# Kernel tuning notes

Hardware: AMD Instinct MI355X
Metric: run time of the kernel (lower is better)

Reference implementation:

```python
import jax, jax.numpy as jnp
import numpy as np

DECAY = 0.99
EPS = 1e-06


def setup_inputs() -> dict:
    key = jax.random.key(0)
    k1, k2, k3 = jax.random.split(key, 3)
    B, S, D, K = 8, 8192, 256, 2048
    x = jax.random.normal(k1, (B, S, D), dtype=jnp.float32)
    embed = jax.random.normal(k2, (K, D), dtype=jnp.float32)
    cluster_size = jnp.ones((K,), dtype=jnp.float32)
    embed_avg = jax.random.normal(k3, (K, D), dtype=jnp.float32)
    return {"x": x, "embed": embed, "cluster_size": cluster_size, "embed_avg": embed_avg}


def reference(x, embed, cluster_size, embed_avg):
    # x: [B, S, D]; embed/embed_avg: [K, D]; cluster_size: [K]
    B, S, D = x.shape
    K = embed.shape[0]
    xf = x.reshape(-1, D)  # [N, D]
    dist = (
        jnp.sum(xf * xf, axis=1, keepdims=True)
        - 2.0 * (xf @ embed.T)
        + jnp.sum(embed * embed, axis=1)
    )
    embed_ind_flat = jnp.argmin(dist, axis=-1)  # [N]
    quantize = embed[embed_ind_flat].reshape(B, S, D)
    embed_ind = embed_ind_flat.reshape(B, S)

    # EMA updates (training branch). one_hot.sum(0) == per-code counts,
    # one_hot.T @ x == per-code feature sums; use segment_sum (no NxK one-hot).
    counts = jax.ops.segment_sum(
        jnp.ones((B * S,), dtype=jnp.float32), embed_ind_flat, num_segments=K
    )
    embed_sum = jax.ops.segment_sum(xf, embed_ind_flat, num_segments=K)  # [K, D]
    new_cluster_size = cluster_size * DECAY + (1.0 - DECAY) * counts
    new_embed_avg = embed_avg * DECAY + (1.0 - DECAY) * embed_sum
    total = new_cluster_size.sum()
    smoothed = (new_cluster_size + EPS) / (total + EPS * K) * total  # laplace smoothing
    new_embed = new_embed_avg / smoothed[:, None]
    return quantize, embed_ind, new_cluster_size, new_embed_avg, new_embed
```

## Files before the change

kernel.cpp:

```cpp
#include <hip/hip_runtime.h>
#include <hip/hip_bf16.h>
#include <float.h>

#define DECAY 0.99f
#define OMD   0.01f
#define EPSF  1e-6f

constexpr int Bb = 8, Ss = 8192, Dd = 256, Kk = 2048;
constexpr int Nn = Bb * Ss;

constexpr long OUT_QUANT = 0;
constexpr long OUT_IND   = (long)Nn * Dd;
constexpr long OUT_NCS   = OUT_IND + Nn;
constexpr long OUT_NEA   = OUT_NCS + Kk;
constexpr long OUT_NE    = OUT_NEA + (long)Kk * Dd;

constexpr long WS_COUNTS = 0;
constexpr long WS_TOTAL  = 2048;
constexpr long WS_EE     = 2112;
constexpr long WS_BIG    = 4160;
constexpr int  PARTS     = 8;

typedef __attribute__((ext_vector_type(8))) short short8;
typedef __attribute__((ext_vector_type(4))) float floatx4;

#define WINDOW 0.0625f

__device__ __forceinline__ void gl_lds(const ushort* g, ushort* l)
{
    __builtin_amdgcn_global_load_lds(
        (const __attribute__((address_space(1))) void*)g,
        (__attribute__((address_space(3))) void*)l,
        16, 0, 0);
}

__global__ __launch_bounds__(256) void convert_x_kernel(
    const float* __restrict__ x, ushort* __restrict__ x_hi, ushort* __restrict__ x_lo)
{
    long base = ((long)blockIdx.x * 256 + threadIdx.x) * 4;
    float4 v = *(const float4*)&x[base];
    float vv[4] = {v.x, v.y, v.z, v.w};
    ushort hh[4], ll[4];
    #pragma unroll
    for (int i = 0; i < 4; ++i) {
        __hip_bfloat16 hb = __float2bfloat16(vv[i]);
        float r = vv[i] - __bfloat162float(hb);
        __hip_bfloat16 lb = __float2bfloat16(r);
        hh[i] = *(ushort*)&hb; ll[i] = *(ushort*)&lb;
    }
    ushort4 h; h.x = hh[0]; h.y = hh[1]; h.z = hh[2]; h.w = hh[3];
    ushort4 l; l.x = ll[0]; l.y = ll[1]; l.z = ll[2]; l.w = ll[3];
    *(ushort4*)&x_hi[base] = h;
    *(ushort4*)&x_lo[base] = l;
}

__global__ __launch_bounds__(256) void convert_e_kernel(
    const float* __restrict__ embed, ushort* __restrict__ e_hi,
    ushort* __restrict__ e_lo, float* __restrict__ ee)
{
    int row  = blockIdx.x * 4 + (threadIdx.x >> 6);
    int lane = threadIdx.x & 63;
    long base = (long)row * Dd + lane * 4;
    float4 v = *(const float4*)&embed[base];
    float vv[4] = {v.x, v.y, v.z, v.w};
    ushort hh[4], ll[4];
    float s = 0.0f;
    #pragma unroll
    for (int i = 0; i < 4; ++i) {
        s += vv[i] * vv[i];
        __hip_bfloat16 hb = __float2bfloat16(vv[i]);
        float r = vv[i] - __bfloat162float(hb);
        __hip_bfloat16 lb = __float2bfloat16(r);
        hh[i] = *(ushort*)&hb; ll[i] = *(ushort*)&lb;
    }
    ushort4 h; h.x = hh[0]; h.y = hh[1]; h.z = hh[2]; h.w = hh[3];
    ushort4 l; l.x = ll[0]; l.y = ll[1]; l.z = ll[2]; l.w = ll[3];
    *(ushort4*)&e_hi[base] = h;
    *(ushort4*)&e_lo[base] = l;
    #pragma unroll
    for (int off = 32; off >= 1; off >>= 1)
        s += __shfl_xor(s, off, 64);
    if (lane == 0) ee[row] = s;
}

__global__ __attribute__((amdgpu_waves_per_eu(2, 2))) __launch_bounds__(256)
void pass1_kernel(
    const ushort* __restrict__ x_hi, const ushort* __restrict__ x_lo,
    const ushort* __restrict__ e_hi, const ushort* __restrict__ e_lo,
    const float* __restrict__ ee, float* __restrict__ ind_out,
    int* __restrict__ qbase)
{
    __shared__ __attribute__((aligned(16))) ushort ah[2][4096];
    __shared__ __attribute__((aligned(16))) ushort al[2][4096];
    __shared__ __attribute__((aligned(16))) ushort bh[2][4096];
    __shared__ __attribute__((aligned(16))) ushort bl[2][4096];
    __shared__ float  redv[2][128];
    __shared__ float  red2[2][128];
    __shared__ int    redi[2][128];

    const int tid  = threadIdx.x;
    const int lane = tid & 63;
    const int quad = lane >> 4;
    const int l15  = lane & 15;
    const int w    = tid >> 6;
    const int wy   = w >> 1;
    const int wx   = w & 1;
    const long row0 = (long)blockIdx.x * 128;

    const int rloc   = lane >> 2;
    const int cchunk = (lane & 3) ^ ((rloc >> 1) & 3);
    const int gcoff  = rloc * 256 + cchunk * 8;

    const int sread = (l15 >> 1) & 3;
    const int aoff0 = ((wy * 64 + l15) << 5) + ((quad ^ sread) << 3);
    const int boff0 = ((wx * 64 + l15) << 5) + ((quad ^ sread) << 3);

    float bestv[16], best2v[16];
    int   besti[16];
    #pragma unroll
    for (int i = 0; i < 16; ++i) { bestv[i] = FLT_MAX; best2v[i] = FLT_MAX; besti[i] = 0; }

#define STAGE(b, ctn, kcn)                                                       \
    do {                                                                         \
        const int  kcol_ = (kcn) * 32;                                           \
        const long brow_ = (long)(ctn) * 128;                                    \
        gl_lds(&x_hi[((row0 + w * 16) << 8) + kcol_ + gcoff],       &ah[b][w * 512]);       \
        gl_lds(&x_hi[((row0 + (w + 4) * 16) << 8) + kcol_ + gcoff], &ah[b][(w + 4) * 512]); \
        gl_lds(&x_lo[((row0 + w * 16) << 8) + kcol_ + gcoff],       &al[b][w * 512]);       \
        gl_lds(&x_lo[((row0 + (w + 4) * 16) << 8) + kcol_ + gcoff], &al[b][(w + 4) * 512]); \
        gl_lds(&e_hi[((brow_ + w * 16) << 8) + kcol_ + gcoff],       &bh[b][w * 512]);       \
        gl_lds(&e_hi[((brow_ + (w + 4) * 16) << 8) + kcol_ + gcoff], &bh[b][(w + 4) * 512]); \
        gl_lds(&e_lo[((brow_ + w * 16) << 8) + kcol_ + gcoff],       &bl[b][w * 512]);       \
        gl_lds(&e_lo[((brow_ + (w + 4) * 16) << 8) + kcol_ + gcoff], &bl[b][(w + 4) * 512]); \
    } while (0)

    STAGE(0, 0, 0);

    for (int ct = 0; ct < 16; ++ct) {
        floatx4 acc[4][4];
        #pragma unroll
        for (int rt = 0; rt < 4; ++rt)
            #pragma unroll
            for (int jt = 0; jt < 4; ++jt)
                acc[rt][jt] = (floatx4){0.f, 0.f, 0.f, 0.f};

        for (int kc = 0; kc < 8; ++kc) {
            const int t   = ct * 8 + kc;
            const int cur = t & 1;
            const int tn  = (t + 1) & 127;

            STAGE(cur ^ 1, tn >> 3, tn & 7);
            asm volatile("s_waitcnt vmcnt(8)" ::: "memory");
            __builtin_amdgcn_s_barrier();
            __builtin_amdgcn_sched_barrier(0);

            short8 afh[4], bfh[4], afl[4], bfl[4];
            #pragma unroll
            for (int rt = 0; rt < 4; ++rt)
                afh[rt] = *(const short8*)&ah[cur][aoff0 + (rt << 9)];
            #pragma unroll
            for (int jt = 0; jt < 4; ++jt)
                bfh[jt] = *(const short8*)&bh[cur][boff0 + (jt << 9)];
            __builtin_amdgcn_s_setprio(1);
            #pragma unroll
            for (int rt = 0; rt < 4; ++rt)
                #pragma unroll
                for (int jt = 0; jt < 4; ++jt)
                    acc[rt][jt] = __builtin_amdgcn_mfma_f32_16x16x32_bf16(
                        afh[rt], bfh[jt], acc[rt][jt], 0, 0, 0);
            __builtin_amdgcn_s_setprio(0);

            #pragma unroll
            for (int rt = 0; rt < 4; ++rt)
                afl[rt] = *(const short8*)&al[cur][aoff0 + (rt << 9)];
            __builtin_amdgcn_s_setprio(1);
            #pragma unroll
            for (int rt = 0; rt < 4; ++rt)
                #pragma unroll
                for (int jt = 0; jt < 4; ++jt)
                    acc[rt][jt] = __builtin_amdgcn_mfma_f32_16x16x32_bf16(
                        afl[rt], bfh[jt], acc[rt][jt], 0, 0, 0);
            __builtin_amdgcn_s_setprio(0);

            #pragma unroll
            for (int jt = 0; jt < 4; ++jt)
                bfl[jt] = *(const short8*)&bl[cur][boff0 + (jt << 9)];
            __builtin_amdgcn_s_setprio(1);
            #pragma unroll
            for (int rt = 0; rt < 4; ++rt)
                #pragma unroll
                for (int jt = 0; jt < 4; ++jt)
                    acc[rt][jt] = __builtin_amdgcn_mfma_f32_16x16x32_bf16(
                        afh[rt], bfl[jt], acc[rt][jt], 0, 0, 0);
            __builtin_amdgcn_s_setprio(0);

            __builtin_amdgcn_sched_barrier(0);
            __builtin_amdgcn_s_barrier();
        }

        #pragma unroll
        for (int jt = 0; jt < 4; ++jt) {
            int c = ct * 128 + wx * 64 + jt * 16 + l15;
            float eec = ee[c];
            #pragma unroll
            for (int rt = 0; rt < 4; ++rt) {
                #pragma unroll
                for (int reg = 0; reg < 4; ++reg) {
                    float s = eec - 2.0f * acc[rt][jt][reg];
                    int slot = rt * 4 + reg;
                    if (s < bestv[slot]) {
                        best2v[slot] = bestv[slot];
                        bestv[slot] = s; besti[slot] = c;
                    } else {
                        best2v[slot] = fminf(best2v[slot], s);
                    }
                }
            }
        }
    }
#undef STAGE
    asm volatile("s_waitcnt vmcnt(0)" ::: "memory");

    #pragma unroll
    for (int slot = 0; slot < 16; ++slot) {
        float bv = bestv[slot]; int bi = besti[slot]; float b2 = best2v[slot];
        #pragma unroll
        for (int off = 8; off >= 1; off >>= 1) {
            float ov  = __shfl_xor(bv, off, 16);
            int   oi  = __shfl_xor(bi, off, 16);
            float ov2 = __shfl_xor(b2, off, 16);
            float nm2 = fminf(fminf(b2, ov2), fmaxf(bv, ov));
            if (ov < bv) { bv = ov; bi = oi; }
            b2 = nm2;
        }
        bestv[slot] = bv; besti[slot] = bi; best2v[slot] = b2;
    }

    if (l15 == 0) {
        #pragma unroll
        for (int rt = 0; rt < 4; ++rt)
            #pragma unroll
            for (int reg = 0; reg < 4; ++reg) {
                int rloc2 = wy * 64 + rt * 16 + quad * 4 + reg;
                int slot = rt * 4 + reg;
                redv[wx][rloc2] = bestv[slot];
                red2[wx][rloc2] = best2v[slot];
                redi[wx][rloc2] = besti[slot];
            }
    }
    __syncthreads();
    if (tid < 128) {
        float v0 = redv[0][tid], v1 = redv[1][tid];
        float s0 = red2[0][tid], s1 = red2[1][tid];
        float m1, m2; int mi;
        if (v0 <= v1) { m1 = v0; mi = redi[0][tid]; m2 = fminf(fminf(s0, s1), v1); }
        else          { m1 = v1; mi = redi[1][tid]; m2 = fminf(fminf(s0, s1), v0); }
        long rowAbs = row0 + tid;
        ind_out[rowAbs] = (float)mi;
        if (m2 - m1 <= WINDOW) {
            int q = atomicAdd(qbase, 1);
            qbase[1 + q] = (int)rowAbs;
        }
    }
}

constexpr int RB = 8;
__global__ __launch_bounds__(256) void pass2_kernel(
    const float* __restrict__ x, const float* __restrict__ embed,
    const float* __restrict__ ee, const int* __restrict__ qbase,
    float* __restrict__ ind_out)
{
    __shared__ float xs[RB][256];
    __shared__ float sv[RB][256];
    __shared__ int   si[RB][256];
    const int tid = threadIdx.x;
    const int count = qbase[0];

    for (int q0 = blockIdx.x * RB; q0 < count; q0 += gridDim.x * RB) {
        const int nr = (count - q0 < RB) ? (count - q0) : RB;
        __syncthreads();
        for (int r = 0; r < nr; ++r)
            xs[r][tid] = x[(long)qbase[1 + q0 + r] * Dd + tid];
        __syncthreads();

        float bv[RB]; int bi[RB];
        #pragma unroll
        for (int r = 0; r < RB; ++r) { bv[r] = FLT_MAX; bi[r] = 0; }

        for (int i = 0; i < Kk / 256; ++i) {
            const int c = i * 256 + tid;
            const float4* er = (const float4*)&embed[(long)c * Dd];
            float dot[RB];
            #pragma unroll
            for (int r = 0; r < RB; ++r) dot[r] = 0.0f;
            for (int d = 0; d < Dd / 4; ++d) {
                float4 e4 = er[d];
                #pragma unroll
                for (int r = 0; r < RB; ++r) {
                    float4 x4 = *(const float4*)&xs[r][d * 4];
                    dot[r] += e4.x * x4.x + e4.y * x4.y + e4.z * x4.z + e4.w * x4.w;
                }
            }
            float eec = ee[c];
            #pragma unroll
            for (int r = 0; r < RB; ++r) {
                float s = eec - 2.0f * dot[r];
                if (s < bv[r]) { bv[r] = s; bi[r] = c; }
            }
        }

        #pragma unroll
        for (int r = 0; r < RB; ++r) { sv[r][tid] = bv[r]; si[r][tid] = bi[r]; }
        __syncthreads();
        for (int off = 128; off >= 1; off >>= 1) {
            if (tid < off) {
                #pragma unroll
                for (int r = 0; r < RB; ++r) {
                    float v2 = sv[r][tid + off]; int i2 = si[r][tid + off];
                    if (v2 < sv[r][tid] || (v2 == sv[r][tid] && i2 < si[r][tid])) {
                        sv[r][tid] = v2; si[r][tid] = i2;
                    }
                }
            }
            __syncthreads();
        }
        if (tid < nr)
            ind_out[qbase[1 + q0 + tid]] = (float)si[tid][0];
        __syncthreads();
    }
}

__global__ __launch_bounds__(256) void quant_gather_kernel(
    const float* __restrict__ embed, const float* __restrict__ ind_f,
    float* __restrict__ quant)
{
    long row  = (long)blockIdx.x * 4 + (threadIdx.x >> 6);
    int  lane = threadIdx.x & 63;
    int  idx  = (int)ind_f[row];
    float4 ev = *(const float4*)&embed[(long)idx * Dd + lane * 4];
    *(float4*)&quant[row * Dd + lane * 4] = ev;
}

template <int USE_ATOMIC>
__global__ __launch_bounds__(256) void segsum_kernel(
    const float* __restrict__ x, const float* __restrict__ ind_f,
    float* __restrict__ dst, float* __restrict__ counts)
{
    __shared__ float part[4][256];
    __shared__ float cnt_l[4];
    const int tid  = threadIdx.x;
    const int w    = tid >> 6;
    const int lane = tid & 63;
    const int k    = blockIdx.x >> 3;
    const int s    = blockIdx.x & 7;

    constexpr int STRIP = Nn / PARTS;
    constexpr int WAVE_ROWS = STRIP / 4;
    const int base0 = s * STRIP + w * WAVE_ROWS;

    float4 acc = {0.f, 0.f, 0.f, 0.f};
    int cnt = 0;
    for (int win = 0; win < WAVE_ROWS; win += 64) {
        int idx = (int)ind_f[base0 + win + lane];
        unsigned long long m = __ballot(idx == k);
        cnt += __popcll(m);
        while (m) {
            int l = __ffsll((unsigned long long)m) - 1;
            m &= m - 1;
            long row = base0 + win + l;
            float4 v = *(const float4*)&x[row * Dd + lane * 4];
            acc.x += v.x; acc.y += v.y; acc.z += v.z; acc.w += v.w;
        }
    }
    *(float4*)&part[w][lane * 4] = acc;
    if (lane == 0) cnt_l[w] = (float)cnt;
    __syncthreads();
    float sum = part[0][tid] + part[1][tid] + part[2][tid] + part[3][tid];
    if (USE_ATOMIC) {
        if (sum != 0.0f) atomicAdd(&dst[(long)k * Dd + tid], sum);
    } else {
        dst[((long)s * Kk + k) * Dd + tid] = sum;
    }
    if (tid == 0)
        atomicAdd(&counts[k], cnt_l[0] + cnt_l[1] + cnt_l[2] + cnt_l[3]);
}

__global__ __launch_bounds__(256) void ema_cs_kernel(
    const float* __restrict__ cs, const float* __restrict__ counts,
    float* __restrict__ ncs, float* __restrict__ total_ws)
{
    __shared__ float red[256];
    int tid = threadIdx.x;
    float s = 0.0f;
    #pragma unroll
    for (int i = 0; i < 8; ++i) {
        int k = tid + i * 256;
        float v = cs[k] * DECAY + OMD * counts[k];
        ncs[k] = v;
        s += v;
    }
    red[tid] = s;
    __syncthreads();
    #pragma unroll
    for (int off = 128; off >= 1; off >>= 1) {
        if (tid < off) red[tid] += red[tid + off];
        __syncthreads();
    }
    if (tid == 0) total_ws[0] = red[0];
}

__global__ __launch_bounds__(256) void nea_ne_kernel(
    const float* __restrict__ ea, const float* __restrict__ partials,
    int nparts, const float* __restrict__ ncs, const float* __restrict__ total_ws,
    float* __restrict__ nea, float* __restrict__ ne)
{
    long g = ((long)blockIdx.x * 256 + threadIdx.x) * 4;
    int  k = (int)(g >> 8);
    int  d = (int)(g & 255);

    float4 sv = {0.f, 0.f, 0.f, 0.f};
    for (int p = 0; p < nparts; ++p) {
        float4 pv = *(const float4*)&partials[((long)p * Kk + k) * Dd + d];
        sv.x += pv.x; sv.y += pv.y; sv.z += pv.z; sv.w += pv.w;
    }

    float4 av = *(const float4*)&ea[g];
    float4 out_nea;
    out_nea.x = av.x * DECAY + OMD * sv.x;
    out_nea.y = av.y * DECAY + OMD * sv.y;
    out_nea.z = av.z * DECAY + OMD * sv.z;
    out_nea.w = av.w * DECAY + OMD * sv.w;
    *(float4*)&nea[g] = out_nea;

    float total = total_ws[0];
    float sm = (ncs[k] + EPSF) / (total + EPSF * (float)Kk) * total;
    float inv = 1.0f / sm;
    float4 out_ne;
    out_ne.x = out_nea.x * inv;
    out_ne.y = out_nea.y * inv;
    out_ne.z = out_nea.z * inv;
    out_ne.w = out_nea.w * inv;
    *(float4*)&ne[g] = out_ne;
}

extern "C" void kernel_launch(void* const* d_in, const int* in_sizes, int n_in,
                              void* d_out, int out_size, void* d_ws, size_t ws_size,
                              hipStream_t stream)
{
    const float* x     = (const float*)d_in[0];
    const float* embed = (const float*)d_in[1];
    const float* cs    = (const float*)d_in[2];
    const float* ea    = (const float*)d_in[3];

    float* out   = (float*)d_out;
    float* quant = out + OUT_QUANT;
    float* ind_f = out + OUT_IND;
    float* ncs   = out + OUT_NCS;
    float* nea   = out + OUT_NEA;
    float* ne    = out + OUT_NE;

    float* ws     = (float*)d_ws;
    float* counts = ws + WS_COUNTS;
    float* total  = ws + WS_TOTAL;
    float* ee     = ws + WS_EE;
    float* big    = ws + WS_BIG;

    ushort* x_hi = (ushort*)(out + OUT_QUANT);
    ushort* x_lo = (ushort*)(out + OUT_QUANT + Nn * (Dd / 2));
    ushort* e_hi = (ushort*)(out + OUT_NEA);
    ushort* e_lo = (ushort*)(out + OUT_NEA + Kk * (Dd / 2));
    int*    qb   = (int*)(out + OUT_NE);

    const size_t need_partials =
        (size_t)(WS_BIG + (long)PARTS * Kk * Dd) * sizeof(float) + 1024;
    const bool use_ws_partials = ws_size >= need_partials;

    hipMemsetAsync(counts, 0, Kk * sizeof(float), stream);
    hipMemsetAsync(qb, 0, sizeof(int), stream);
    if (!use_ws_partials)
        hipMemsetAsync(big, 0, (size_t)Kk * Dd * sizeof(float), stream);

    convert_x_kernel<<<(Nn * Dd / 4) / 256, 256, 0, stream>>>(x, x_hi, x_lo);
    convert_e_kernel<<<Kk / 4, 256, 0, stream>>>(embed, e_hi, e_lo, ee);
    pass1_kernel<<<Nn / 128, 256, 0, stream>>>(x_hi, x_lo, e_hi, e_lo, ee, ind_f, qb);
    pass2_kernel<<<256, 256, 0, stream>>>(x, embed, ee, qb, ind_f);
    quant_gather_kernel<<<Nn / 4, 256, 0, stream>>>(embed, ind_f, quant);
    if (use_ws_partials)
        segsum_kernel<0><<<Kk * PARTS, 256, 0, stream>>>(x, ind_f, big, counts);
    else
        segsum_kernel<1><<<Kk * PARTS, 256, 0, stream>>>(x, ind_f, big, counts);
    ema_cs_kernel<<<1, 256, 0, stream>>>(cs, counts, ncs, total);
    nea_ne_kernel<<<(Kk * Dd / 4) / 256, 256, 0, stream>>>(
        ea, big, use_ws_partials ? PARTS : 1, ncs, total, nea, ne);
}
```

Before: 542.4 us.

## Widen pass1 code tile to 256 and batch eight codes per segsum block

pass1 now processes 256 codebook columns per tile with a single LDS buffer and plain syncthreads instead of the double-buffered 128-column async pipeline, so each x tile is reused across more MFMAs. The segment-sum kernel handles eight codes per block, scanning the index array once per group of eight codes instead of once per code, which cuts the redundant index reads by a factor of eight. The tradeoff is that global loads in pass1 are no longer overlapped with compute, and the larger accumulator array raises register pressure.

```diff
diff --git a/kernel.cpp b/kernel.cpp
--- a/kernel.cpp
+++ b/kernel.cpp
@@ -20,6 +20,7 @@
 constexpr long WS_EE     = 2112;
 constexpr long WS_BIG    = 4160;
 constexpr int  PARTS     = 8;
+constexpr int  CODES     = 8;
 
 typedef __attribute__((ext_vector_type(8))) short short8;
 typedef __attribute__((ext_vector_type(4))) float floatx4;
@@ -90,10 +91,10 @@
     const float* __restrict__ ee, float* __restrict__ ind_out,
     int* __restrict__ qbase)
 {
-    __shared__ __attribute__((aligned(16))) ushort ah[2][4096];
-    __shared__ __attribute__((aligned(16))) ushort al[2][4096];
-    __shared__ __attribute__((aligned(16))) ushort bh[2][4096];
-    __shared__ __attribute__((aligned(16))) ushort bl[2][4096];
+    __shared__ __attribute__((aligned(16))) ushort ah[128 * 32];
+    __shared__ __attribute__((aligned(16))) ushort al[128 * 32];
+    __shared__ __attribute__((aligned(16))) ushort bh[256 * 32];
+    __shared__ __attribute__((aligned(16))) ushort bl[256 * 32];
     __shared__ float  redv[2][128];
     __shared__ float  red2[2][128];
     __shared__ int    redi[2][128];
@@ -113,94 +114,69 @@
 
     const int sread = (l15 >> 1) & 3;
     const int aoff0 = ((wy * 64 + l15) << 5) + ((quad ^ sread) << 3);
-    const int boff0 = ((wx * 64 + l15) << 5) + ((quad ^ sread) << 3);
+    const int boff0 = ((wx * 128 + l15) << 5) + ((quad ^ sread) << 3);
 
     float bestv[16], best2v[16];
     int   besti[16];
     #pragma unroll
     for (int i = 0; i < 16; ++i) { bestv[i] = FLT_MAX; best2v[i] = FLT_MAX; besti[i] = 0; }
 
-#define STAGE(b, ctn, kcn)                                                       \
-    do {                                                                         \
-        const int  kcol_ = (kcn) * 32;                                           \
-        const long brow_ = (long)(ctn) * 128;                                    \
-        gl_lds(&x_hi[((row0 + w * 16) << 8) + kcol_ + gcoff],       &ah[b][w * 512]);       \
-        gl_lds(&x_hi[((row0 + (w + 4) * 16) << 8) + kcol_ + gcoff], &ah[b][(w + 4) * 512]); \
-        gl_lds(&x_lo[((row0 + w * 16) << 8) + kcol_ + gcoff],       &al[b][w * 512]);       \
-        gl_lds(&x_lo[((row0 + (w + 4) * 16) << 8) + kcol_ + gcoff], &al[b][(w + 4) * 512]); \
-        gl_lds(&e_hi[((brow_ + w * 16) << 8) + kcol_ + gcoff],       &bh[b][w * 512]);       \
-        gl_lds(&e_hi[((brow_ + (w + 4) * 16) << 8) + kcol_ + gcoff], &bh[b][(w + 4) * 512]); \
-        gl_lds(&e_lo[((brow_ + w * 16) << 8) + kcol_ + gcoff],       &bl[b][w * 512]);       \
-        gl_lds(&e_lo[((brow_ + (w + 4) * 16) << 8) + kcol_ + gcoff], &bl[b][(w + 4) * 512]); \
-    } while (0)
-
-    STAGE(0, 0, 0);
-
-    for (int ct = 0; ct < 16; ++ct) {
-        floatx4 acc[4][4];
+    for (int ct = 0; ct < Kk / 256; ++ct) {
+        floatx4 acc[4][8];
         #pragma unroll
         for (int rt = 0; rt < 4; ++rt)
             #pragma unroll
-            for (int jt = 0; jt < 4; ++jt)
+            for (int jt = 0; jt < 8; ++jt)
                 acc[rt][jt] = (floatx4){0.f, 0.f, 0.f, 0.f};
 
+        const long brow = (long)ct * 256;
+
         for (int kc = 0; kc < 8; ++kc) {
-            const int t   = ct * 8 + kc;
-            const int cur = t & 1;
-            const int tn  = (t + 1) & 127;
-
-            STAGE(cur ^ 1, tn >> 3, tn & 7);
-            asm volatile("s_waitcnt vmcnt(8)" ::: "memory");
-            __builtin_amdgcn_s_barrier();
-            __builtin_amdgcn_sched_barrier(0);
-
-            short8 afh[4], bfh[4], afl[4], bfl[4];
+            const int kcol = kc * 32;
+
+            __syncthreads();
+            gl_lds(&x_hi[((row0 + w * 16) << 8) + kcol + gcoff],       &ah[w * 512]);
+            gl_lds(&x_hi[((row0 + (w + 4) * 16) << 8) + kcol + gcoff], &ah[(w + 4) * 512]);
+            gl_lds(&x_lo[((row0 + w * 16) << 8) + kcol + gcoff],       &al[w * 512]);
+            gl_lds(&x_lo[((row0 + (w + 4) * 16) << 8) + kcol + gcoff], &al[(w + 4) * 512]);
+            #pragma unroll
+            for (int i = 0; i < 4; ++i) {
+                const int seg = w + 4 * i;
+                gl_lds(&e_hi[((brow + seg * 16) << 8) + kcol + gcoff], &bh[seg * 512]);
+                gl_lds(&e_lo[((brow + seg * 16) << 8) + kcol + gcoff], &bl[seg * 512]);
+            }
+            __syncthreads();
+
+            short8 afh[4], afl[4];
             #pragma unroll
             for (int rt = 0; rt < 4; ++rt)
-                afh[rt] = *(const short8*)&ah[cur][aoff0 + (rt << 9)];
-            #pragma unroll
-            for (int jt = 0; jt < 4; ++jt)
-                bfh[jt] = *(const short8*)&bh[cur][boff0 + (jt << 9)];
-            __builtin_amdgcn_s_setprio(1);
+                afh[rt] = *(const short8*)&ah[aoff0 + (rt << 9)];
             #pragma unroll
             for (int rt = 0; rt < 4; ++rt)
-                #pragma unroll
-                for (int jt = 0; jt < 4; ++jt)
+                afl[rt] = *(const short8*)&al[aoff0 + (rt << 9)];
+
+            #pragma unroll
+            for (int jt = 0; jt < 8; ++jt) {
+                short8 bfh = *(const short8*)&bh[boff0 + (jt << 9)];
+                short8 bfl = *(const short8*)&bl[boff0 + (jt << 9)];
+                #pragma unroll
+                for (int rt = 0; rt < 4; ++rt)
                     acc[rt][jt] = __builtin_amdgcn_mfma_f32_16x16x32_bf16(
-                        afh[rt], bfh[jt], acc[rt][jt], 0, 0, 0);
-            __builtin_amdgcn_s_setprio(0);
-
-            #pragma unroll
-            for (int rt = 0; rt < 4; ++rt)
-                afl[rt] = *(const short8*)&al[cur][aoff0 + (rt << 9)];
-            __builtin_amdgcn_s_setprio(1);
-            #pragma unroll
-            for (int rt = 0; rt < 4; ++rt)
-                #pragma unroll
-                for (int jt = 0; jt < 4; ++jt)
+                        afh[rt], bfh, acc[rt][jt], 0, 0, 0);
+                #pragma unroll
+                for (int rt = 0; rt < 4; ++rt)
                     acc[rt][jt] = __builtin_amdgcn_mfma_f32_16x16x32_bf16(
-                        afl[rt], bfh[jt], acc[rt][jt], 0, 0, 0);
-            __builtin_amdgcn_s_setprio(0);
-
-            #pragma unroll
-            for (int jt = 0; jt < 4; ++jt)
-                bfl[jt] = *(const short8*)&bl[cur][boff0 + (jt << 9)];
-            __builtin_amdgcn_s_setprio(1);
-            #pragma unroll
-            for (int rt = 0; rt < 4; ++rt)
-                #pragma unroll
-                for (int jt = 0; jt < 4; ++jt)
+                        afl[rt], bfh, acc[rt][jt], 0, 0, 0);
+                #pragma unroll
+                for (int rt = 0; rt < 4; ++rt)
                     acc[rt][jt] = __builtin_amdgcn_mfma_f32_16x16x32_bf16(
-                        afh[rt], bfl[jt], acc[rt][jt], 0, 0, 0);
-            __builtin_amdgcn_s_setprio(0);
-
-            __builtin_amdgcn_sched_barrier(0);
-            __builtin_amdgcn_s_barrier();
-        }
-
-        #pragma unroll
-        for (int jt = 0; jt < 4; ++jt) {
-            int c = ct * 128 + wx * 64 + jt * 16 + l15;
+                        afh[rt], bfl, acc[rt][jt], 0, 0, 0);
+            }
+        }
+
+        #pragma unroll
+        for (int jt = 0; jt < 8; ++jt) {
+            int c = ct * 256 + wx * 128 + jt * 16 + l15;
             float eec = ee[c];
             #pragma unroll
             for (int rt = 0; rt < 4; ++rt) {
@@ -218,8 +194,6 @@
             }
         }
     }
-#undef STAGE
-    asm volatile("s_waitcnt vmcnt(0)" ::: "memory");
 
     #pragma unroll
     for (int slot = 0; slot < 16; ++slot) {
@@ -346,43 +320,65 @@
     const float* __restrict__ x, const float* __restrict__ ind_f,
     float* __restrict__ dst, float* __restrict__ counts)
 {
-    __shared__ float part[4][256];
-    __shared__ float cnt_l[4];
+    __shared__ float part[CODES][4][256];
+    __shared__ float cnt_l[CODES][4];
     const int tid  = threadIdx.x;
     const int w    = tid >> 6;
     const int lane = tid & 63;
-    const int k    = blockIdx.x >> 3;
+    const int k0   = (blockIdx.x >> 3) * CODES;
     const int s    = blockIdx.x & 7;
 
     constexpr int STRIP = Nn / PARTS;
     constexpr int WAVE_ROWS = STRIP / 4;
     const int base0 = s * STRIP + w * WAVE_ROWS;
 
-    float4 acc = {0.f, 0.f, 0.f, 0.f};
-    int cnt = 0;
+    float4 acc[CODES];
+    int    cnt[CODES];
+    #pragma unroll
+    for (int c = 0; c < CODES; ++c) { acc[c] = (float4){0.f,0.f,0.f,0.f}; cnt[c] = 0; }
+
     for (int win = 0; win < WAVE_ROWS; win += 64) {
         int idx = (int)ind_f[base0 + win + lane];
-        unsigned long long m = __ballot(idx == k);
-        cnt += __popcll(m);
+        unsigned rel = (unsigned)(idx - k0);
+        unsigned long long m = __ballot(rel < (unsigned)CODES);
         while (m) {
             int l = __ffsll((unsigned long long)m) - 1;
             m &= m - 1;
+            int code = __shfl((int)rel, l, 64);
             long row = base0 + win + l;
             float4 v = *(const float4*)&x[row * Dd + lane * 4];
-            acc.x += v.x; acc.y += v.y; acc.z += v.z; acc.w += v.w;
-        }
-    }
-    *(float4*)&part[w][lane * 4] = acc;
-    if (lane == 0) cnt_l[w] = (float)cnt;
+            switch (code) {
+                case 0: acc[0].x+=v.x; acc[0].y+=v.y; acc[0].z+=v.z; acc[0].w+=v.w; cnt[0]++; break;
+                case 1: acc[1].x+=v.x; acc[1].y+=v.y; acc[1].z+=v.z; acc[1].w+=v.w; cnt[1]++; break;
+                case 2: acc[2].x+=v.x; acc[2].y+=v.y; acc[2].z+=v.z; acc[2].w+=v.w; cnt[2]++; break;
+                case 3: acc[3].x+=v.x; acc[3].y+=v.y; acc[3].z+=v.z; acc[3].w+=v.w; cnt[3]++; break;
+                case 4: acc[4].x+=v.x; acc[4].y+=v.y; acc[4].z+=v.z; acc[4].w+=v.w; cnt[4]++; break;
+                case 5: acc[5].x+=v.x; acc[5].y+=v.y; acc[5].z+=v.z; acc[5].w+=v.w; cnt[5]++; break;
+                case 6: acc[6].x+=v.x; acc[6].y+=v.y; acc[6].z+=v.z; acc[6].w+=v.w; cnt[6]++; break;
+                case 7: acc[7].x+=v.x; acc[7].y+=v.y; acc[7].z+=v.z; acc[7].w+=v.w; cnt[7]++; break;
+            }
+        }
+    }
+
+    #pragma unroll
+    for (int c = 0; c < CODES; ++c) {
+        *(float4*)&part[c][w][lane * 4] = acc[c];
+        if (lane == 0) cnt_l[c][w] = (float)cnt[c];
+    }
     __syncthreads();
-    float sum = part[0][tid] + part[1][tid] + part[2][tid] + part[3][tid];
-    if (USE_ATOMIC) {
-        if (sum != 0.0f) atomicAdd(&dst[(long)k * Dd + tid], sum);
-    } else {
-        dst[((long)s * Kk + k) * Dd + tid] = sum;
-    }
-    if (tid == 0)
-        atomicAdd(&counts[k], cnt_l[0] + cnt_l[1] + cnt_l[2] + cnt_l[3]);
+
+    #pragma unroll
+    for (int c = 0; c < CODES; ++c) {
+        float sum = part[c][0][tid] + part[c][1][tid] + part[c][2][tid] + part[c][3][tid];
+        if (USE_ATOMIC) {
+            if (sum != 0.0f) atomicAdd(&dst[(long)(k0 + c) * Dd + tid], sum);
+        } else {
+            dst[((long)s * Kk + (k0 + c)) * Dd + tid] = sum;
+        }
+    }
+    if (tid < CODES)
+        atomicAdd(&counts[k0 + tid],
+                  cnt_l[tid][0] + cnt_l[tid][1] + cnt_l[tid][2] + cnt_l[tid][3]);
 }
 
 __global__ __launch_bounds__(256) void ema_cs_kernel(
@@ -486,9 +482,9 @@
     pass2_kernel<<<256, 256, 0, stream>>>(x, embed, ee, qb, ind_f);
     quant_gather_kernel<<<Nn / 4, 256, 0, stream>>>(embed, ind_f, quant);
     if (use_ws_partials)
-        segsum_kernel<0><<<Kk * PARTS, 256, 0, stream>>>(x, ind_f, big, counts);
+        segsum_kernel<0><<<(Kk / CODES) * PARTS, 256, 0, stream>>>(x, ind_f, big, counts);
     else
-        segsum_kernel<1><<<Kk * PARTS, 256, 0, stream>>>(x, ind_f, big, counts);
+        segsum_kernel<1><<<(Kk / CODES) * PARTS, 256, 0, stream>>>(x, ind_f, big, counts);
     ema_cs_kernel<<<1, 256, 0, stream>>>(cs, counts, ncs, total);
     nea_ne_kernel<<<(Kk * Dd / 4) / 256, 256, 0, stream>>>(
         ea, big, use_ws_partials ? PARTS : 1, ncs, total, nea, ne);
```

Measured after the change: 487.6 us. 10.1% less time.
